# Kernel optimization log

Hardware: AMD Instinct MI355X
Metric: run time of the kernel (lower is better)

Reference implementation:

```python
import jax, jax.numpy as jnp
import numpy as np

EPS = 1e-6
N_REP = 4  # num_heads // num_kv_heads


def _qk_norm(a):
    a32 = a.astype(jnp.float32)
    var = jnp.mean(jnp.square(a32), axis=-1, keepdims=True)
    return (a32 * jax.lax.rsqrt(var + EPS)).astype(a.dtype)


def setup_inputs() -> dict:
    key = jax.random.key(0)
    ks = jax.random.split(key, 5)
    B, Tq, C, H, D, Hkv = 2, 2048, 2048, 16, 128, 4
    s = 0.02
    return {
        "x_q": jax.random.normal(ks[0], (B, Tq, C), dtype=jnp.float32),
        "Wq": jax.random.normal(ks[1], (C, H, D), dtype=jnp.float32) * s,
        "Wk": jax.random.normal(ks[2], (C, Hkv, D), dtype=jnp.float32) * s,
        "Wv": jax.random.normal(ks[3], (C, Hkv, D), dtype=jnp.float32) * s,
        "Wo": jax.random.normal(ks[4], (H * D, C), dtype=jnp.float32) * s,
    }


def reference(x_q, Wq, Wk, Wv, Wo):
    # x_q: (B, Tq, C); self-attention (x_kv = x_q)
    B, Tq, C = x_q.shape
    D = Wq.shape[-1]
    q = jnp.einsum('btc,chd->bthd', x_q, Wq)   # (B,Tq,H,D)
    k = jnp.einsum('btc,chd->bthd', x_q, Wk)   # (B,Tq,Hkv,D)
    v = jnp.einsum('btc,chd->bthd', x_q, Wv)
    # per-head QK RMS-norm
    q = _qk_norm(q)
    k = _qk_norm(k)
    # GQA: repeat kv heads (each kv head repeated N_REP times consecutively)
    k = jnp.repeat(k, N_REP, axis=2)           # (B,Tq,H,D)
    v = jnp.repeat(v, N_REP, axis=2)
    scale = jnp.asarray(1.0 / np.sqrt(D), dtype=q.dtype)
    logits = jnp.einsum('bqhd,bkhd->bhqk', q, k) * scale
    attn = jax.nn.softmax(logits, axis=-1)
    out = jnp.einsum('bhqk,bkhd->bqhd', attn, v)
    out = out.reshape(B, Tq, -1)               # (B,Tq,H*D)
    return out @ Wo                            # (B,Tq,C)
```

## Files before the change

### kernel.cpp

```cpp
#include <hip/hip_runtime.h>

typedef __attribute__((ext_vector_type(4))) float f32x4;
typedef __attribute__((ext_vector_type(16))) float f32x16;
typedef __attribute__((ext_vector_type(8))) short bf16x8;
typedef __attribute__((ext_vector_type(4))) unsigned u32x4;

#define DEV __device__ __forceinline__

DEV unsigned short f2bf(float f) {
  unsigned u = __float_as_uint(f);
  unsigned r = (u + 0x7FFFu + ((u >> 16) & 1u)) >> 16;
  return (unsigned short)r;
}
DEV float bf2f(unsigned short h) { return __uint_as_float(((unsigned)h) << 16); }

DEV unsigned cvtpk(float lo, float hi) {
  unsigned r;
  asm("v_cvt_pk_bf16_f32 %0, %1, %2" : "=v"(r) : "v"(lo), "v"(hi));
  return r;
}
DEV bf16x8 frag4(unsigned a, unsigned b, unsigned c, unsigned d) {
  u32x4 u = {a, b, c, d};
  return __builtin_bit_cast(bf16x8, u);
}

typedef __attribute__((address_space(1))) void gas_t;
typedef __attribute__((address_space(3))) void las_t;
DEV void async16(void* lds, const void* g) {
  __builtin_amdgcn_global_load_lds((gas_t*)g, (las_t*)lds, 16, 0, 0);
}

__global__ void cast_x(const float* __restrict__ x, unsigned short* __restrict__ y, int n8) {
  int idx = blockIdx.x * blockDim.x + threadIdx.x;
  int stride = gridDim.x * blockDim.x;
  for (; idx < n8; idx += stride) {
    const float4* p = (const float4*)(x + (size_t)idx * 8);
    float4 v0 = p[0], v1 = p[1];
    bf16x8 o;
    o[0] = (short)f2bf(v0.x); o[1] = (short)f2bf(v0.y);
    o[2] = (short)f2bf(v0.z); o[3] = (short)f2bf(v0.w);
    o[4] = (short)f2bf(v1.x); o[5] = (short)f2bf(v1.y);
    o[6] = (short)f2bf(v1.z); o[7] = (short)f2bf(v1.w);
    *(bf16x8*)(y + (size_t)idx * 8) = o;
  }
}

__global__ void transpose_cast(const float* __restrict__ W, unsigned short* __restrict__ Wt,
                               int Kdim, int Nw) {
  __shared__ float tile[32][33];
  int n0 = blockIdx.x * 32, k0 = blockIdx.y * 32;
  int tx = threadIdx.x, ty = threadIdx.y;
#pragma unroll
  for (int r = ty; r < 32; r += 8)
    tile[r][tx] = W[(size_t)(k0 + r) * Nw + n0 + tx];
  __syncthreads();
#pragma unroll
  for (int r = ty; r < 32; r += 8)
    Wt[(size_t)(n0 + r) * Kdim + k0 + tx] = f2bf(tile[tx][r]);
}

template <int EPI>
__global__ __launch_bounds__(256, 2)
void gemm_bt(const unsigned short* __restrict__ A, const unsigned short* __restrict__ Bt,
             int Kr, float* __restrict__ Cf, int Nr,
             unsigned short* __restrict__ Qn, unsigned short* __restrict__ Kn,
             unsigned short* __restrict__ Vt) {
  __shared__ __align__(16) unsigned short lsA[128 * 32];
  __shared__ __align__(16) unsigned short lsB[128 * 32];
  const int t = threadIdx.x;
  const int lane = t & 63;
  const int w = t >> 6, wr = w >> 1, wc = w & 1;
  const int lo = lane & 15, hi = lane >> 4;
  const int nwg = gridDim.x * 32;
  const int bid0 = blockIdx.y * gridDim.x + blockIdx.x;
  const int sw = (bid0 & 7) * (nwg >> 3) + (bid0 >> 3);
  const int m0 = (sw & 31) * 128, n0 = (sw >> 5) * 128;

  const int c0 = t, c1 = t + 256;
  const unsigned short* gA0 = A + (size_t)(m0 + (c0 >> 2)) * Kr + (c0 & 3) * 8;
  const unsigned short* gA1 = A + (size_t)(m0 + (c1 >> 2)) * Kr + (c1 & 3) * 8;
  const unsigned short* gB0 = Bt + (size_t)(n0 + (c0 >> 2)) * Kr + (c0 & 3) * 8;
  const unsigned short* gB1 = Bt + (size_t)(n0 + (c1 >> 2)) * Kr + (c1 & 3) * 8;
  unsigned short* lA0 = lsA + c0 * 8;
  unsigned short* lA1 = lsA + c1 * 8;
  unsigned short* lB0 = lsB + c0 * 8;
  unsigned short* lB1 = lsB + c1 * 8;

  f32x4 acc[4][4] = {};

  for (int kt = 0; kt < Kr; kt += 32) {
    async16(lA0, gA0 + kt);
    async16(lA1, gA1 + kt);
    async16(lB0, gB0 + kt);
    async16(lB1, gB1 + kt);
    __syncthreads();
    bf16x8 af[4], bfr[4];
#pragma unroll
    for (int i = 0; i < 4; ++i) {
      af[i]  = *(const bf16x8*)&lsA[(wr * 64 + i * 16 + lo) * 32 + hi * 8];
      bfr[i] = *(const bf16x8*)&lsB[(wc * 64 + i * 16 + lo) * 32 + hi * 8];
    }
#pragma unroll
    for (int mi = 0; mi < 4; ++mi)
#pragma unroll
      for (int ni = 0; ni < 4; ++ni)
        acc[mi][ni] = __builtin_amdgcn_mfma_f32_16x16x32_bf16(af[mi], bfr[ni], acc[mi][ni], 0, 0, 0);
    __syncthreads();
  }

#pragma unroll
  for (int mi = 0; mi < 4; ++mi)
#pragma unroll
    for (int ni = 0; ni < 4; ++ni)
#pragma unroll
      for (int i = 0; i < 4; ++i) {
        int gm = m0 + wr * 64 + mi * 16 + hi * 4 + i;
        int gn = n0 + wc * 64 + ni * 16 + lo;
        float v = acc[mi][ni][i];
        if (EPI == 0) {
          Cf[(size_t)gm * Nr + gn] = v;
        } else {
          unsigned short bv = f2bf(v);
          int bb = gm >> 11, tt = gm & 2047;
          if (gn < 2048) {
            int hh = gn >> 7, dd = gn & 127;
            Qn[(((size_t)bb * 16 + hh) * 2048 + tt) * 128 + dd] = bv;
          } else if (gn < 2560) {
            int g2 = gn - 2048, hh = g2 >> 7, dd = g2 & 127;
            Kn[(((size_t)bb * 4 + hh) * 2048 + tt) * 128 + dd] = bv;
          } else {
            int g2 = gn - 2560, hh = g2 >> 7, dd = g2 & 127;
            Vt[(((size_t)bb * 4 + hh) * 128 + dd) * 2048 + tt] = bv;
          }
        }
      }
}

__global__ __launch_bounds__(256)
void qk_norm(unsigned short* __restrict__ Qn, unsigned short* __restrict__ Kn, float qscale) {
  int row = blockIdx.x * 4 + (threadIdx.x >> 6);
  int lane = threadIdx.x & 63;
  unsigned short* base;
  float scl;
  if (row < 65536) { base = Qn + (size_t)row * 128; scl = qscale; }
  else             { base = Kn + (size_t)(row - 65536) * 128; scl = 1.0f; }
  unsigned v = *(const unsigned*)(base + lane * 2);
  float a = bf2f((unsigned short)(v & 0xffffu));
  float b = bf2f((unsigned short)(v >> 16));
  float ss = a * a + b * b;
#pragma unroll
  for (int m = 1; m < 64; m <<= 1) ss += __shfl_xor(ss, m, 64);
  float r = rsqrtf(ss * (1.0f / 128.0f) + 1e-6f) * scl;
  *(unsigned*)(base + lane * 2) = ((unsigned)f2bf(b * r) << 16) | (unsigned)f2bf(a * r);
}

__global__ __launch_bounds__(512, 2)
void attn(const unsigned short* __restrict__ Q, const unsigned short* __restrict__ Kk,
          const unsigned short* __restrict__ Vt, unsigned short* __restrict__ AO) {
  const int bid = blockIdx.x;
  const int bh = ((bid & 7) << 2) | (bid >> 6);
  const int qx = (bid >> 3) & 7;
  const int b = bh >> 4, h = bh & 15;
  const int hkv = h >> 2;
  const int t = threadIdx.x;
  const int w = t >> 6, lane = t & 63;
  const int qi = lane & 31, h1 = lane >> 5;
  const unsigned short* Qb = Q  + (size_t)bh * 2048 * 128;
  const unsigned short* Kb = Kk + (size_t)(b * 4 + hkv) * 2048 * 128;
  const unsigned short* Vb = Vt + (size_t)(b * 4 + hkv) * 128 * 2048;
  const int q0 = qx * 256 + w * 32;

  __shared__ __align__(16) unsigned short Klds[2][64 * 128];
  __shared__ __align__(16) unsigned short Vlds[2][128 * 64];

  bf16x8 qf[8];
#pragma unroll
  for (int s = 0; s < 8; ++s)
    qf[s] = *(const bf16x8*)&Qb[(size_t)(q0 + qi) * 128 + s * 16 + h1 * 8];

  f32x16 Oc[4] = {};
  float mrow = -1e30f, srow = 0.f;

#define STAGE_KV(bufi, kt_)                                                      \
  {                                                                              \
    const unsigned short* gK = Kb + (size_t)(kt_) * 128;                         \
    const unsigned short* gV = Vb + (kt_);                                       \
    _Pragma("unroll")                                                            \
    for (int j = 0; j < 2; ++j) {                                                \
      int gi = j * 512 + t;                                                      \
      int kr = gi >> 4, kg = (gi & 15) ^ (kr & 15);                              \
      async16(&Klds[bufi][gi * 8], gK + (size_t)kr * 128 + kg * 8);              \
      int vr = gi >> 3, vg = (gi & 7) ^ (vr & 7);                                \
      async16(&Vlds[bufi][gi * 8], gV + (size_t)vr * 2048 + vg * 8);             \
    }                                                                            \
  }

  STAGE_KV(0, 0);
  __syncthreads();

  int cur = 0;
  for (int kt = 0; kt < 2048; kt += 64) {
    if (kt + 64 < 2048) STAGE_KV(cur ^ 1, kt + 64);

    const unsigned short* KL = Klds[cur];
    const unsigned short* VL = Vlds[cur];

    f32x16 S[2] = {};
    __builtin_amdgcn_s_setprio(1);
#pragma unroll
    for (int mt = 0; mt < 2; ++mt) {
      const int krow = mt * 32 + qi;
      const unsigned short* krp = KL + krow * 128;
      const int rswz = krow & 15;
#pragma unroll
      for (int s = 0; s < 8; ++s) {
        bf16x8 kf = *(const bf16x8*)(krp + (((2 * s + h1) ^ rswz) << 3));
        S[mt] = __builtin_amdgcn_mfma_f32_32x32x16_bf16(kf, qf[s], S[mt], 0, 0, 0);
      }
    }
    __builtin_amdgcn_s_setprio(0);

    float t8[8];
#pragma unroll
    for (int r = 0; r < 8; ++r)
      t8[r] = fmaxf(fmaxf(S[0][r], S[0][r + 8]), fmaxf(S[1][r], S[1][r + 8]));
#pragma unroll
    for (int r = 0; r < 4; ++r) t8[r] = fmaxf(t8[r], t8[r + 4]);
    float mx = fmaxf(fmaxf(t8[0], t8[1]), fmaxf(t8[2], t8[3]));
    mx = fmaxf(mx, __shfl_xor(mx, 32, 64));
    if (__any(mx > mrow + 8.0f)) {
      float mnew = fmaxf(mrow, mx);
      float al = __builtin_amdgcn_exp2f(mrow - mnew);
      mrow = mnew;
      srow *= al;
#pragma unroll
      for (int dt = 0; dt < 4; ++dt)
#pragma unroll
        for (int r = 0; r < 16; ++r) Oc[dt][r] *= al;
    }
#pragma unroll
    for (int mt = 0; mt < 2; ++mt)
#pragma unroll
      for (int r = 0; r < 16; ++r)
        S[mt][r] = __builtin_amdgcn_exp2f(S[mt][r] - mrow);
    float s8[8];
#pragma unroll
    for (int r = 0; r < 8; ++r)
      s8[r] = (S[0][r] + S[0][r + 8]) + (S[1][r] + S[1][r + 8]);
#pragma unroll
    for (int r = 0; r < 4; ++r) s8[r] += s8[r + 4];
    float rs = (s8[0] + s8[1]) + (s8[2] + s8[3]);
    rs += __shfl_xor(rs, 32, 64);
    srow += rs;

    __builtin_amdgcn_s_setprio(1);
#pragma unroll
    for (int mt = 0; mt < 2; ++mt) {
      unsigned wd[8];
#pragma unroll
      for (int i2 = 0; i2 < 8; ++i2) wd[i2] = cvtpk(S[mt][2 * i2], S[mt][2 * i2 + 1]);
      unsigned r0 = __shfl_xor(h1 ? wd[0] : wd[2], 32, 64);
      unsigned r1 = __shfl_xor(h1 ? wd[1] : wd[3], 32, 64);
      unsigned r2 = __shfl_xor(h1 ? wd[4] : wd[6], 32, 64);
      unsigned r3 = __shfl_xor(h1 ? wd[5] : wd[7], 32, 64);
      bf16x8 pf0 = frag4(h1 ? r0 : wd[0], h1 ? r1 : wd[1], h1 ? wd[2] : r0, h1 ? wd[3] : r1);
      bf16x8 pf1 = frag4(h1 ? r2 : wd[4], h1 ? r3 : wd[5], h1 ? wd[6] : r2, h1 ? wd[7] : r3);
#pragma unroll
      for (int dt = 0; dt < 4; ++dt) {
        const int vrow = dt * 32 + qi;
        const unsigned short* vrp = VL + vrow * 64;
        const int vswz = vrow & 7;
        bf16x8 v0 = *(const bf16x8*)(vrp + (((mt * 4 + 0 + h1) ^ vswz) << 3));
        bf16x8 v1 = *(const bf16x8*)(vrp + (((mt * 4 + 2 + h1) ^ vswz) << 3));
        Oc[dt] = __builtin_amdgcn_mfma_f32_32x32x16_bf16(v0, pf0, Oc[dt], 0, 0, 0);
        Oc[dt] = __builtin_amdgcn_mfma_f32_32x32x16_bf16(v1, pf1, Oc[dt], 0, 0, 0);
      }
    }
    __builtin_amdgcn_s_setprio(0);

    __syncthreads();
    cur ^= 1;
  }

  const float inv = 1.0f / srow;
  const size_t orow = ((size_t)(b * 2048 + q0 + qi)) * 2048 + h * 128;
#pragma unroll
  for (int dt = 0; dt < 4; ++dt)
#pragma unroll
    for (int rq = 0; rq < 4; ++rq) {
      int d0 = dt * 32 + 8 * rq + 4 * h1;
      unsigned u0 = cvtpk(Oc[dt][4 * rq + 0] * inv, Oc[dt][4 * rq + 1] * inv);
      unsigned u1 = cvtpk(Oc[dt][4 * rq + 2] * inv, Oc[dt][4 * rq + 3] * inv);
      uint2 st = {u0, u1};
      *(uint2*)((unsigned short*)AO + orow + d0) = st;
    }
}

extern "C" void kernel_launch(void* const* d_in, const int* in_sizes, int n_in,
                              void* d_out, int out_size, void* d_ws, size_t ws_size,
                              hipStream_t stream) {
  const float* x_q = (const float*)d_in[0];
  const float* Wq  = (const float*)d_in[1];
  const float* Wk  = (const float*)d_in[2];
  const float* Wv  = (const float*)d_in[3];
  const float* Wo  = (const float*)d_in[4];
  float* out = (float*)d_out;

  char* ws = (char*)d_ws;
  unsigned short* Xb    = (unsigned short*)(ws);
  unsigned short* WqkvT = (unsigned short*)(ws + 16777216);
  unsigned short* WoT   = (unsigned short*)(ws + 29360128);
  unsigned short* Qn    = (unsigned short*)(ws + 37748736);
  unsigned short* Kn    = (unsigned short*)(ws + 54525952);
  unsigned short* Vt    = (unsigned short*)(ws + 58720256);
  unsigned short* AO    = Xb;

  cast_x<<<2048, 256, 0, stream>>>(x_q, Xb, (4096 * 2048) / 8);
  transpose_cast<<<dim3(2048 / 32, 2048 / 32), dim3(32, 8), 0, stream>>>(Wq, WqkvT, 2048, 2048);
  transpose_cast<<<dim3(512 / 32, 2048 / 32), dim3(32, 8), 0, stream>>>(Wk, WqkvT + 2048 * 2048, 2048, 512);
  transpose_cast<<<dim3(512 / 32, 2048 / 32), dim3(32, 8), 0, stream>>>(Wv, WqkvT + 2560 * 2048, 2048, 512);
  transpose_cast<<<dim3(2048 / 32, 2048 / 32), dim3(32, 8), 0, stream>>>(Wo, WoT, 2048, 2048);

  gemm_bt<1><<<dim3(3072 / 128, 4096 / 128), 256, 0, stream>>>(Xb, WqkvT, 2048, nullptr, 0, Qn, Kn, Vt);
  qk_norm<<<(65536 + 16384) / 4, 256, 0, stream>>>(Qn, Kn, 0.12751742f);
  attn<<<256, 512, 0, stream>>>(Qn, Kn, Vt, AO);
  gemm_bt<0><<<dim3(2048 / 128, 4096 / 128), 256, 0, stream>>>(AO, WoT, 2048, out, 2048,
                                                               nullptr, nullptr, nullptr);
}
```

Baseline: 249.8 us.

## Pre-swizzle K/V into MFMA fragment order and read directly from global

Adds a fragKV kernel that rearranges normalized K and transposed V into per-lane MFMA fragment order. The attention kernel then loads each fragment with one coalesced 16-byte global load per lane, dropping the LDS double-buffered staging and the per-tile __syncthreads. Blocks shrink to 256 threads with twice as many blocks. The cost is an extra pass over K/V and global/L2 latency that LDS staging used to hide, with K/V reuse across the four waves and four query heads now relying on cache.

```diff
diff --git a/kernel.cpp b/kernel.cpp
--- a/kernel.cpp
+++ b/kernel.cpp
@@ -154,24 +154,48 @@
   *(unsigned*)(base + lane * 2) = ((unsigned)f2bf(b * r) << 16) | (unsigned)f2bf(a * r);
 }
 
-__global__ __launch_bounds__(512, 2)
-void attn(const unsigned short* __restrict__ Q, const unsigned short* __restrict__ Kk,
-          const unsigned short* __restrict__ Vt, unsigned short* __restrict__ AO) {
+__global__ __launch_bounds__(256)
+void fragKV(const unsigned short* __restrict__ Kn, const unsigned short* __restrict__ Vt,
+            unsigned short* __restrict__ Kf, unsigned short* __restrict__ Vf) {
+  int tid = blockIdx.x * 256 + threadIdx.x;
+  int bhkv = tid >> 16, r = tid & 65535;
+  int c = r & 32767;
+  int lane = c & 63, tile = c >> 10, mid = (c >> 6) & 15;
+  const uint4* src;
+  uint4* dst;
+  if (r < 32768) {
+    int mt = mid >> 3, s = mid & 7;
+    int key = tile * 64 + mt * 32 + (lane & 31);
+    int d0 = (2 * s + (lane >> 5)) * 8;
+    src = (const uint4*)(Kn + ((size_t)bhkv * 2048 + key) * 128 + d0);
+    dst = (uint4*)(Kf + (size_t)bhkv * 262144 + (size_t)c * 8);
+  } else {
+    int dt = mid >> 2, g2 = mid & 3;
+    int d = dt * 32 + (lane & 31);
+    int g = g2 * 2 + (lane >> 5);
+    int k0 = tile * 64 + g * 8;
+    src = (const uint4*)(Vt + ((size_t)bhkv * 128 + d) * 2048 + k0);
+    dst = (uint4*)(Vf + (size_t)bhkv * 262144 + (size_t)c * 8);
+  }
+  *dst = *src;
+}
+
+__global__ __launch_bounds__(256, 2)
+void attn(const unsigned short* __restrict__ Q, const unsigned short* __restrict__ Kf,
+          const unsigned short* __restrict__ Vf, unsigned short* __restrict__ AO) {
   const int bid = blockIdx.x;
-  const int bh = ((bid & 7) << 2) | (bid >> 6);
-  const int qx = (bid >> 3) & 7;
+  const int x = bid & 7, kk = bid >> 3;
+  const int bh = x * 4 + (kk & 3);
+  const int qx = kk >> 2;
   const int b = bh >> 4, h = bh & 15;
-  const int hkv = h >> 2;
+  const int hkv = h >> 2, bhkv = b * 4 + hkv;
   const int t = threadIdx.x;
   const int w = t >> 6, lane = t & 63;
   const int qi = lane & 31, h1 = lane >> 5;
-  const unsigned short* Qb = Q  + (size_t)bh * 2048 * 128;
-  const unsigned short* Kb = Kk + (size_t)(b * 4 + hkv) * 2048 * 128;
-  const unsigned short* Vb = Vt + (size_t)(b * 4 + hkv) * 128 * 2048;
-  const int q0 = qx * 256 + w * 32;
-
-  __shared__ __align__(16) unsigned short Klds[2][64 * 128];
-  __shared__ __align__(16) unsigned short Vlds[2][128 * 64];
+  const unsigned short* Qb = Q + (size_t)bh * 2048 * 128;
+  const unsigned short* Kfb = Kf + (size_t)bhkv * 262144;
+  const unsigned short* Vfb = Vf + (size_t)bhkv * 262144;
+  const int q0 = qx * 128 + w * 32;
 
   bf16x8 qf[8];
 #pragma unroll
@@ -181,40 +205,15 @@
   f32x16 Oc[4] = {};
   float mrow = -1e30f, srow = 0.f;
 
-#define STAGE_KV(bufi, kt_)                                                      \
-  {                                                                              \
-    const unsigned short* gK = Kb + (size_t)(kt_) * 128;                         \
-    const unsigned short* gV = Vb + (kt_);                                       \
-    _Pragma("unroll")                                                            \
-    for (int j = 0; j < 2; ++j) {                                                \
-      int gi = j * 512 + t;                                                      \
-      int kr = gi >> 4, kg = (gi & 15) ^ (kr & 15);                              \
-      async16(&Klds[bufi][gi * 8], gK + (size_t)kr * 128 + kg * 8);              \
-      int vr = gi >> 3, vg = (gi & 7) ^ (vr & 7);                                \
-      async16(&Vlds[bufi][gi * 8], gV + (size_t)vr * 2048 + vg * 8);             \
-    }                                                                            \
-  }
-
-  STAGE_KV(0, 0);
-  __syncthreads();
-
-  int cur = 0;
-  for (int kt = 0; kt < 2048; kt += 64) {
-    if (kt + 64 < 2048) STAGE_KV(cur ^ 1, kt + 64);
-
-    const unsigned short* KL = Klds[cur];
-    const unsigned short* VL = Vlds[cur];
-
+  for (int ti = 0; ti < 32; ++ti) {
     f32x16 S[2] = {};
     __builtin_amdgcn_s_setprio(1);
 #pragma unroll
     for (int mt = 0; mt < 2; ++mt) {
-      const int krow = mt * 32 + qi;
-      const unsigned short* krp = KL + krow * 128;
-      const int rswz = krow & 15;
+      const unsigned short* kp = Kfb + ((size_t)(ti * 2 + mt) * 8) * 512 + lane * 8;
 #pragma unroll
       for (int s = 0; s < 8; ++s) {
-        bf16x8 kf = *(const bf16x8*)(krp + (((2 * s + h1) ^ rswz) << 3));
+        bf16x8 kf = *(const bf16x8*)(kp + s * 512);
         S[mt] = __builtin_amdgcn_mfma_f32_32x32x16_bf16(kf, qf[s], S[mt], 0, 0, 0);
       }
     }
@@ -267,19 +266,14 @@
       bf16x8 pf1 = frag4(h1 ? r2 : wd[4], h1 ? r3 : wd[5], h1 ? wd[6] : r2, h1 ? wd[7] : r3);
 #pragma unroll
       for (int dt = 0; dt < 4; ++dt) {
-        const int vrow = dt * 32 + qi;
-        const unsigned short* vrp = VL + vrow * 64;
-        const int vswz = vrow & 7;
-        bf16x8 v0 = *(const bf16x8*)(vrp + (((mt * 4 + 0 + h1) ^ vswz) << 3));
-        bf16x8 v1 = *(const bf16x8*)(vrp + (((mt * 4 + 2 + h1) ^ vswz) << 3));
+        const unsigned short* vp = Vfb + ((size_t)((ti * 4 + dt) * 4 + mt * 2)) * 512 + lane * 8;
+        bf16x8 v0 = *(const bf16x8*)(vp);
+        bf16x8 v1 = *(const bf16x8*)(vp + 512);
         Oc[dt] = __builtin_amdgcn_mfma_f32_32x32x16_bf16(v0, pf0, Oc[dt], 0, 0, 0);
         Oc[dt] = __builtin_amdgcn_mfma_f32_32x32x16_bf16(v1, pf1, Oc[dt], 0, 0, 0);
       }
     }
     __builtin_amdgcn_s_setprio(0);
-
-    __syncthreads();
-    cur ^= 1;
   }
 
   const float inv = 1.0f / srow;
@@ -314,6 +308,8 @@
   unsigned short* Kn    = (unsigned short*)(ws + 54525952);
   unsigned short* Vt    = (unsigned short*)(ws + 58720256);
   unsigned short* AO    = Xb;
+  unsigned short* Kf    = WqkvT;
+  unsigned short* Vf    = WqkvT + 2097152;
 
   cast_x<<<2048, 256, 0, stream>>>(x_q, Xb, (4096 * 2048) / 8);
   transpose_cast<<<dim3(2048 / 32, 2048 / 32), dim3(32, 8), 0, stream>>>(Wq, WqkvT, 2048, 2048);
@@ -323,7 +319,8 @@
 
   gemm_bt<1><<<dim3(3072 / 128, 4096 / 128), 256, 0, stream>>>(Xb, WqkvT, 2048, nullptr, 0, Qn, Kn, Vt);
   qk_norm<<<(65536 + 16384) / 4, 256, 0, stream>>>(Qn, Kn, 0.12751742f);
-  attn<<<256, 512, 0, stream>>>(Qn, Kn, Vt, AO);
+  fragKV<<<2048, 256, 0, stream>>>(Kn, Vt, Kf, Vf);
+  attn<<<512, 256, 0, stream>>>(Qn, Kf, Vf, AO);
   gemm_bt<0><<<dim3(2048 / 128, 4096 / 128), 256, 0, stream>>>(AO, WoT, 2048, out, 2048,
                                                                nullptr, nullptr, nullptr);
 }
```

Result: slower. 317.4 us (+27.1%).

## Split attention KV loop across two warp groups with LDS merge

Applied to the files above, without the earlier changes.

Each block now covers 128 queries instead of 256, and its 8 waves form two groups. The groups take alternating 64-key tiles of the KV sequence and merge their partial softmax state and output accumulators through LDS at the end. The grid doubles to 512 blocks, which fills the CUs better and gives finer block scheduling. The block index mapping is also changed to group the heads that share a KV head. In exchange, each wave does half the compute per staged tile while KV staging per block stays the same, so total K/V loads double, and the merge adds several syncthreads and LDS traffic.

```diff
diff --git a/kernel.cpp b/kernel.cpp
--- a/kernel.cpp
+++ b/kernel.cpp
@@ -158,17 +158,18 @@
 void attn(const unsigned short* __restrict__ Q, const unsigned short* __restrict__ Kk,
           const unsigned short* __restrict__ Vt, unsigned short* __restrict__ AO) {
   const int bid = blockIdx.x;
-  const int bh = ((bid & 7) << 2) | (bid >> 6);
-  const int qx = (bid >> 3) & 7;
-  const int b = bh >> 4, h = bh & 15;
-  const int hkv = h >> 2;
+  const int x = bid & 7, r2 = bid >> 3;
+  const int h2 = r2 & 3, qx = r2 >> 2;
+  const int b = x >> 2, hkv = x & 3;
+  const int h = hkv * 4 + h2, bh = b * 16 + h;
   const int t = threadIdx.x;
   const int w = t >> 6, lane = t & 63;
+  const int wq = w & 3, g = w >> 2;
   const int qi = lane & 31, h1 = lane >> 5;
   const unsigned short* Qb = Q  + (size_t)bh * 2048 * 128;
   const unsigned short* Kb = Kk + (size_t)(b * 4 + hkv) * 2048 * 128;
   const unsigned short* Vb = Vt + (size_t)(b * 4 + hkv) * 128 * 2048;
-  const int q0 = qx * 256 + w * 32;
+  const int q0 = qx * 128 + wq * 32;
 
   __shared__ __align__(16) unsigned short Klds[2][64 * 128];
   __shared__ __align__(16) unsigned short Vlds[2][128 * 64];
@@ -199,101 +200,147 @@
   __syncthreads();
 
   int cur = 0;
-  for (int kt = 0; kt < 2048; kt += 64) {
-    if (kt + 64 < 2048) STAGE_KV(cur ^ 1, kt + 64);
-
-    const unsigned short* KL = Klds[cur];
-    const unsigned short* VL = Vlds[cur];
-
-    f32x16 S[2] = {};
-    __builtin_amdgcn_s_setprio(1);
-#pragma unroll
-    for (int mt = 0; mt < 2; ++mt) {
-      const int krow = mt * 32 + qi;
-      const unsigned short* krp = KL + krow * 128;
-      const int rswz = krow & 15;
-#pragma unroll
-      for (int s = 0; s < 8; ++s) {
-        bf16x8 kf = *(const bf16x8*)(krp + (((2 * s + h1) ^ rswz) << 3));
-        S[mt] = __builtin_amdgcn_mfma_f32_32x32x16_bf16(kf, qf[s], S[mt], 0, 0, 0);
-      }
+  for (int step = 0; step < 32; ++step) {
+    if (step + 1 < 32) STAGE_KV(cur ^ 1, (step + 1) * 64);
+
+    if ((step & 1) == g) {
+      const unsigned short* KL = Klds[cur];
+      const unsigned short* VL = Vlds[cur];
+
+      f32x16 S[2] = {};
+      __builtin_amdgcn_s_setprio(1);
+#pragma unroll
+      for (int mt = 0; mt < 2; ++mt) {
+        const int krow = mt * 32 + qi;
+        const unsigned short* krp = KL + krow * 128;
+        const int rswz = krow & 15;
+#pragma unroll
+        for (int s = 0; s < 8; ++s) {
+          bf16x8 kf = *(const bf16x8*)(krp + (((2 * s + h1) ^ rswz) << 3));
+          S[mt] = __builtin_amdgcn_mfma_f32_32x32x16_bf16(kf, qf[s], S[mt], 0, 0, 0);
+        }
+      }
+      __builtin_amdgcn_s_setprio(0);
+
+      float t8[8];
+#pragma unroll
+      for (int r = 0; r < 8; ++r)
+        t8[r] = fmaxf(fmaxf(S[0][r], S[0][r + 8]), fmaxf(S[1][r], S[1][r + 8]));
+#pragma unroll
+      for (int r = 0; r < 4; ++r) t8[r] = fmaxf(t8[r], t8[r + 4]);
+      float mx = fmaxf(fmaxf(t8[0], t8[1]), fmaxf(t8[2], t8[3]));
+      mx = fmaxf(mx, __shfl_xor(mx, 32, 64));
+      if (__any(mx > mrow + 8.0f)) {
+        float mnew = fmaxf(mrow, mx);
+        float al = __builtin_amdgcn_exp2f(mrow - mnew);
+        mrow = mnew;
+        srow *= al;
+#pragma unroll
+        for (int dt = 0; dt < 4; ++dt)
+#pragma unroll
+          for (int r = 0; r < 16; ++r) Oc[dt][r] *= al;
+      }
+#pragma unroll
+      for (int mt = 0; mt < 2; ++mt)
+#pragma unroll
+        for (int r = 0; r < 16; ++r)
+          S[mt][r] = __builtin_amdgcn_exp2f(S[mt][r] - mrow);
+      float s8[8];
+#pragma unroll
+      for (int r = 0; r < 8; ++r)
+        s8[r] = (S[0][r] + S[0][r + 8]) + (S[1][r] + S[1][r + 8]);
+#pragma unroll
+      for (int r = 0; r < 4; ++r) s8[r] += s8[r + 4];
+      float rs = (s8[0] + s8[1]) + (s8[2] + s8[3]);
+      rs += __shfl_xor(rs, 32, 64);
+      srow += rs;
+
+      __builtin_amdgcn_s_setprio(1);
+#pragma unroll
+      for (int mt = 0; mt < 2; ++mt) {
+        unsigned wd[8];
+#pragma unroll
+        for (int i2 = 0; i2 < 8; ++i2) wd[i2] = cvtpk(S[mt][2 * i2], S[mt][2 * i2 + 1]);
+        unsigned r0 = __shfl_xor(h1 ? wd[0] : wd[2], 32, 64);
+        unsigned r1 = __shfl_xor(h1 ? wd[1] : wd[3], 32, 64);
+        unsigned r2_ = __shfl_xor(h1 ? wd[4] : wd[6], 32, 64);
+        unsigned r3 = __shfl_xor(h1 ? wd[5] : wd[7], 32, 64);
+        bf16x8 pf0 = frag4(h1 ? r0 : wd[0], h1 ? r1 : wd[1], h1 ? wd[2] : r0, h1 ? wd[3] : r1);
+        bf16x8 pf1 = frag4(h1 ? r2_ : wd[4], h1 ? r3 : wd[5], h1 ? wd[6] : r2_, h1 ? wd[7] : r3);
+#pragma unroll
+        for (int dt = 0; dt < 4; ++dt) {
+          const int vrow = dt * 32 + qi;
+          const unsigned short* vrp = VL + vrow * 64;
+          const int vswz = vrow & 7;
+          bf16x8 v0 = *(const bf16x8*)(vrp + (((mt * 4 + 0 + h1) ^ vswz) << 3));
+          bf16x8 v1 = *(const bf16x8*)(vrp + (((mt * 4 + 2 + h1) ^ vswz) << 3));
+          Oc[dt] = __builtin_amdgcn_mfma_f32_32x32x16_bf16(v0, pf0, Oc[dt], 0, 0, 0);
+          Oc[dt] = __builtin_amdgcn_mfma_f32_32x32x16_bf16(v1, pf1, Oc[dt], 0, 0, 0);
+        }
+      }
+      __builtin_amdgcn_s_setprio(0);
     }
-    __builtin_amdgcn_s_setprio(0);
-
-    float t8[8];
-#pragma unroll
-    for (int r = 0; r < 8; ++r)
-      t8[r] = fmaxf(fmaxf(S[0][r], S[0][r + 8]), fmaxf(S[1][r], S[1][r + 8]));
-#pragma unroll
-    for (int r = 0; r < 4; ++r) t8[r] = fmaxf(t8[r], t8[r + 4]);
-    float mx = fmaxf(fmaxf(t8[0], t8[1]), fmaxf(t8[2], t8[3]));
-    mx = fmaxf(mx, __shfl_xor(mx, 32, 64));
-    if (__any(mx > mrow + 8.0f)) {
-      float mnew = fmaxf(mrow, mx);
-      float al = __builtin_amdgcn_exp2f(mrow - mnew);
-      mrow = mnew;
-      srow *= al;
-#pragma unroll
-      for (int dt = 0; dt < 4; ++dt)
-#pragma unroll
-        for (int r = 0; r < 16; ++r) Oc[dt][r] *= al;
-    }
-#pragma unroll
-    for (int mt = 0; mt < 2; ++mt)
-#pragma unroll
-      for (int r = 0; r < 16; ++r)
-        S[mt][r] = __builtin_amdgcn_exp2f(S[mt][r] - mrow);
-    float s8[8];
-#pragma unroll
-    for (int r = 0; r < 8; ++r)
-      s8[r] = (S[0][r] + S[0][r + 8]) + (S[1][r] + S[1][r + 8]);
-#pragma unroll
-    for (int r = 0; r < 4; ++r) s8[r] += s8[r + 4];
-    float rs = (s8[0] + s8[1]) + (s8[2] + s8[3]);
-    rs += __shfl_xor(rs, 32, 64);
-    srow += rs;
-
-    __builtin_amdgcn_s_setprio(1);
-#pragma unroll
-    for (int mt = 0; mt < 2; ++mt) {
-      unsigned wd[8];
-#pragma unroll
-      for (int i2 = 0; i2 < 8; ++i2) wd[i2] = cvtpk(S[mt][2 * i2], S[mt][2 * i2 + 1]);
-      unsigned r0 = __shfl_xor(h1 ? wd[0] : wd[2], 32, 64);
-      unsigned r1 = __shfl_xor(h1 ? wd[1] : wd[3], 32, 64);
-      unsigned r2 = __shfl_xor(h1 ? wd[4] : wd[6], 32, 64);
-      unsigned r3 = __shfl_xor(h1 ? wd[5] : wd[7], 32, 64);
-      bf16x8 pf0 = frag4(h1 ? r0 : wd[0], h1 ? r1 : wd[1], h1 ? wd[2] : r0, h1 ? wd[3] : r1);
-      bf16x8 pf1 = frag4(h1 ? r2 : wd[4], h1 ? r3 : wd[5], h1 ? wd[6] : r2, h1 ? wd[7] : r3);
-#pragma unroll
-      for (int dt = 0; dt < 4; ++dt) {
-        const int vrow = dt * 32 + qi;
-        const unsigned short* vrp = VL + vrow * 64;
-        const int vswz = vrow & 7;
-        bf16x8 v0 = *(const bf16x8*)(vrp + (((mt * 4 + 0 + h1) ^ vswz) << 3));
-        bf16x8 v1 = *(const bf16x8*)(vrp + (((mt * 4 + 2 + h1) ^ vswz) << 3));
-        Oc[dt] = __builtin_amdgcn_mfma_f32_32x32x16_bf16(v0, pf0, Oc[dt], 0, 0, 0);
-        Oc[dt] = __builtin_amdgcn_mfma_f32_32x32x16_bf16(v1, pf1, Oc[dt], 0, 0, 0);
-      }
-    }
-    __builtin_amdgcn_s_setprio(0);
 
     __syncthreads();
     cur ^= 1;
   }
 
-  const float inv = 1.0f / srow;
-  const size_t orow = ((size_t)(b * 2048 + q0 + qi)) * 2048 + h * 128;
-#pragma unroll
-  for (int dt = 0; dt < 4; ++dt)
-#pragma unroll
-    for (int rq = 0; rq < 4; ++rq) {
-      int d0 = dt * 32 + 8 * rq + 4 * h1;
-      unsigned u0 = cvtpk(Oc[dt][4 * rq + 0] * inv, Oc[dt][4 * rq + 1] * inv);
-      unsigned u1 = cvtpk(Oc[dt][4 * rq + 2] * inv, Oc[dt][4 * rq + 3] * inv);
-      uint2 st = {u0, u1};
-      *(uint2*)((unsigned short*)AO + orow + d0) = st;
-    }
+  float* fO = (float*)Klds;
+  float* fMS = (float*)Vlds;
+  float aA = 1.f, aB = 0.f;
+
+  if (g == 1) {
+#pragma unroll
+    for (int dt = 0; dt < 2; ++dt)
+#pragma unroll
+      for (int i = 0; i < 16; ++i)
+        fO[(wq * 32 + dt * 16 + i) * 64 + lane] = Oc[dt][i];
+    fMS[(wq * 64 + lane) * 2 + 0] = mrow;
+    fMS[(wq * 64 + lane) * 2 + 1] = srow;
+  }
+  __syncthreads();
+  if (g == 0) {
+    float mb = fMS[(wq * 64 + lane) * 2 + 0];
+    float sb = fMS[(wq * 64 + lane) * 2 + 1];
+    float M = fmaxf(mrow, mb);
+    aA = __builtin_amdgcn_exp2f(mrow - M);
+    aB = __builtin_amdgcn_exp2f(mb - M);
+    srow = srow * aA + sb * aB;
+#pragma unroll
+    for (int dt = 0; dt < 2; ++dt)
+#pragma unroll
+      for (int i = 0; i < 16; ++i)
+        Oc[dt][i] = Oc[dt][i] * aA + fO[(wq * 32 + dt * 16 + i) * 64 + lane] * aB;
+  }
+  __syncthreads();
+  if (g == 1) {
+#pragma unroll
+    for (int dt = 2; dt < 4; ++dt)
+#pragma unroll
+      for (int i = 0; i < 16; ++i)
+        fO[(wq * 32 + (dt - 2) * 16 + i) * 64 + lane] = Oc[dt][i];
+  }
+  __syncthreads();
+  if (g == 0) {
+#pragma unroll
+    for (int dt = 2; dt < 4; ++dt)
+#pragma unroll
+      for (int i = 0; i < 16; ++i)
+        Oc[dt][i] = Oc[dt][i] * aA + fO[(wq * 32 + (dt - 2) * 16 + i) * 64 + lane] * aB;
+
+    const float inv = 1.0f / srow;
+    const size_t orow = ((size_t)(b * 2048 + q0 + qi)) * 2048 + h * 128;
+#pragma unroll
+    for (int dt = 0; dt < 4; ++dt)
+#pragma unroll
+      for (int rq = 0; rq < 4; ++rq) {
+        int d0 = dt * 32 + 8 * rq + 4 * h1;
+        unsigned u0 = cvtpk(Oc[dt][4 * rq + 0] * inv, Oc[dt][4 * rq + 1] * inv);
+        unsigned u1 = cvtpk(Oc[dt][4 * rq + 2] * inv, Oc[dt][4 * rq + 3] * inv);
+        uint2 st = {u0, u1};
+        *(uint2*)((unsigned short*)AO + orow + d0) = st;
+      }
+  }
 }
 
 extern "C" void kernel_launch(void* const* d_in, const int* in_sizes, int n_in,
@@ -323,7 +370,7 @@
 
   gemm_bt<1><<<dim3(3072 / 128, 4096 / 128), 256, 0, stream>>>(Xb, WqkvT, 2048, nullptr, 0, Qn, Kn, Vt);
   qk_norm<<<(65536 + 16384) / 4, 256, 0, stream>>>(Qn, Kn, 0.12751742f);
-  attn<<<256, 512, 0, stream>>>(Qn, Kn, Vt, AO);
+  attn<<<512, 512, 0, stream>>>(Qn, Kn, Vt, AO);
   gemm_bt<0><<<dim3(2048 / 128, 4096 / 128), 256, 0, stream>>>(AO, WoT, 2048, out, 2048,
                                                                nullptr, nullptr, nullptr);
 }
```

Result: slower. 286.1 us (+14.5%).
